# Kernel tuning notes

Hardware: AMD Instinct MI355X
Metric: run time of the kernel (lower is better)

## Reference

```python
import jax, jax.numpy as jnp
import numpy as np

# Model dims (GatedAttentionLayer of Qwen3.5 ANE hybrid stack)
C = 2048      # hidden_size
H = 16        # num_attention_heads
HK = 4        # num_key_value_heads
D = 128       # head_dim
ROT = 32      # rotary_dim = head_dim * partial_rotary_factor (0.25)
S = 1024      # sequence length (prefill)
CTX = 1024    # kv cache context length
N_ATTN = 6    # number of full-attention layers -> kv_cache leading dim 2*N_ATTN
EPS = 1e-6
ROPE_THETA = 1e7


def _rotate_half(x):
    h = x.shape[-1] // 2
    return jnp.concatenate([-x[..., h:], x[..., :h]], axis=-1)


def _rms_norm(x, w, eps=EPS):
    # Qwen3.5 convention: stored weight is (w - 1), applied as (1 + weight)
    r = jax.lax.rsqrt(jnp.mean(x * x, axis=-1, keepdims=True) + eps)
    return x * r * (1.0 + w)


def setup_inputs() -> dict:
    key = jax.random.key(0)
    ks = jax.random.split(key, 6)
    hidden_states = jax.random.normal(ks[0], (1, C, 1, S), jnp.float32)
    q_proj_w = jax.random.normal(ks[1], (H * 2 * D, C), jnp.float32) * 0.02  # q + gate
    k_proj_w = jax.random.normal(ks[2], (HK * D, C), jnp.float32) * 0.02
    v_proj_w = jax.random.normal(ks[3], (HK * D, C), jnp.float32) * 0.02
    o_proj_w = jax.random.normal(ks[4], (C, H * D), jnp.float32) * 0.02
    q_norm_w = jnp.zeros((D,), jnp.float32)
    k_norm_w = jnp.zeros((D,), jnp.float32)
    kv_cache = jnp.zeros((2 * N_ATTN, HK, CTX, D), jnp.float32)
    position_ids = jnp.arange(S, dtype=jnp.int32)
    # causal mask: 0 on/below diagonal, -1e9 above
    causal_mask = jnp.where(
        jnp.arange(CTX)[None, :] <= jnp.arange(S)[:, None], 0.0, -1e9
    ).astype(jnp.float32)[None, None]  # [1,1,S,CTX]
    # RoPE tables over rotary_dim
    inv_freq = 1.0 / (ROPE_THETA ** (jnp.arange(0, ROT, 2, dtype=jnp.float32) / ROT))
    t = jnp.arange(CTX, dtype=jnp.float32)
    freqs = jnp.outer(t, inv_freq)          # [CTX, ROT//2]
    emb = jnp.concatenate([freqs, freqs], -1)  # [CTX, ROT]
    cos_cached = jnp.cos(emb)
    sin_cached = jnp.sin(emb)
    return dict(hidden_states=hidden_states, q_proj_w=q_proj_w, k_proj_w=k_proj_w,
                v_proj_w=v_proj_w, o_proj_w=o_proj_w, q_norm_w=q_norm_w,
                k_norm_w=k_norm_w, kv_cache=kv_cache, causal_mask=causal_mask,
                position_ids=position_ids, cos_cached=cos_cached,
                sin_cached=sin_cached, attn_layer_idx=0)


def reference(hidden_states, q_proj_w, k_proj_w, v_proj_w, o_proj_w,
              q_norm_w, k_norm_w, kv_cache, causal_mask, position_ids,
              cos_cached, sin_cached, attn_layer_idx):
    x = hidden_states[0, :, 0, :]                     # [C, S]
    q_raw = q_proj_w @ x                              # [H*2D, S]  (1x1 Conv2d == GEMM)
    qg = q_raw.reshape(H, 2 * D, S)
    q = jnp.transpose(qg[:, :D, :], (0, 2, 1))        # [H, S, D]
    gate = jnp.transpose(qg[:, D:, :], (0, 2, 1))     # [H, S, D]
    k = jnp.transpose((k_proj_w @ x).reshape(HK, D, S), (0, 2, 1))  # [HK, S, D]
    v = jnp.transpose((v_proj_w @ x).reshape(HK, D, S), (0, 2, 1))  # [HK, S, D]

    q = _rms_norm(q, q_norm_w)
    k = _rms_norm(k, k_norm_w)

    cos = cos_cached[position_ids]   # [S, ROT]
    sin = sin_cached[position_ids]

    def rope(t):
        rot, pas = t[..., :ROT], t[..., ROT:]
        rot = rot * cos + _rotate_half(rot) * sin
        return jnp.concatenate([rot, pas], axis=-1)

    q, k = rope(q), rope(k)

    # prefill cache write at pos_start = position_ids[0]
    k_idx = 2 * attn_layer_idx
    v_idx = k_idx + 1
    pos_start = position_ids[0]
    kv_cache = jax.lax.dynamic_update_slice(kv_cache, k[None], (k_idx, 0, pos_start, 0))
    kv_cache = jax.lax.dynamic_update_slice(kv_cache, v[None], (v_idx, 0, pos_start, 0))

    g = H // HK  # GQA repeat (expand+reshape == contiguous repeat)
    k_full = jnp.repeat(kv_cache[k_idx], g, axis=0)   # [H, CTX, D]
    v_full = jnp.repeat(kv_cache[v_idx], g, axis=0)   # [H, CTX, D]

    scale = D ** -0.5
    attn = jnp.einsum('hsd,htd->hst', q, k_full) * scale + causal_mask[0]
    attn = jax.nn.softmax(attn, axis=-1)
    out = jnp.einsum('hst,htd->hsd', attn, v_full)    # [H, S, D]
    out = out * jax.nn.sigmoid(gate)
    out = jnp.transpose(out, (0, 2, 1)).reshape(H * D, S)
    output = (o_proj_w @ out)[None, :, None, :]       # [1, C, 1, S]
    return output
```

## Files before the change

kernel.cpp:

```cpp
#include <hip/hip_runtime.h>
#include <cstdint>

#define S_LEN 1024
#define C_DIM 2048
#define NH    16
#define NHK   4
#define HD    128
#define ROT   32
#define SCALE 0.08838834764831845f

typedef __bf16 bf16x8 __attribute__((ext_vector_type(8)));
typedef float floatx4 __attribute__((ext_vector_type(4)));
typedef float floatx16 __attribute__((ext_vector_type(16)));
typedef unsigned short ushortx8 __attribute__((ext_vector_type(8)));

__device__ __forceinline__ unsigned short f2bf(float f) {
  union { float f; uint32_t u; } x; x.f = f;
  uint32_t r = (x.u + 0x7fffu + ((x.u >> 16) & 1u)) >> 16;
  return (unsigned short)r;
}
__device__ __forceinline__ float bf2f(unsigned short v) {
  union { uint32_t u; float f; } x; x.u = (uint32_t)v << 16; return x.f;
}

__device__ __forceinline__ void async_copy16(const unsigned short* g, unsigned short* l) {
  __builtin_amdgcn_global_load_lds(
      (const __attribute__((address_space(1))) void*)g,
      (__attribute__((address_space(3))) void*)l,
      16, 0, 0);
}

__global__ void cast_all_kernel(const float* __restrict__ qw, const float* __restrict__ kw,
                                const float* __restrict__ vw, const float* __restrict__ ow,
                                unsigned short* __restrict__ out) {
  const int NQ = 4096 * 2048 / 4, NK = 512 * 2048 / 4, NV = 512 * 2048 / 4;
  int i = blockIdx.x * blockDim.x + threadIdx.x;
  const float* src; int j;
  if (i < NQ) { src = qw; j = i; }
  else if (i < NQ + NK) { src = kw; j = i - NQ; }
  else if (i < NQ + NK + NV) { src = vw; j = i - NQ - NK; }
  else { src = ow; j = i - NQ - NK - NV; }
  float4 v = ((const float4*)src)[j];
  ushort4 o;
  o.x = f2bf(v.x); o.y = f2bf(v.y); o.z = f2bf(v.z); o.w = f2bf(v.w);
  ((ushort4*)out)[i] = o;
}

__global__ __launch_bounds__(256)
void transpose_cast_x_kernel(const float* __restrict__ x, unsigned short* __restrict__ xT) {
  __shared__ float t[32][33];
  int st = blockIdx.x, ct = blockIdx.y;
  int c = threadIdx.x & 31, rq = threadIdx.x >> 5;
#pragma unroll
  for (int i = 0; i < 4; ++i) {
    int r = rq + i * 8;
    t[r][c] = x[(size_t)(ct * 32 + r) * S_LEN + st * 32 + c];
  }
  __syncthreads();
#pragma unroll
  for (int i = 0; i < 4; ++i) {
    int r = rq + i * 8;
    xT[(size_t)(st * 32 + r) * C_DIM + ct * 32 + c] = f2bf(t[c][r]);
  }
}

__device__ __forceinline__ void norm_rope_epi(
    floatx16 (&acc)[2], float (*pp)[32],
    const float* __restrict__ w, const int* __restrict__ pos_ids,
    const float* __restrict__ cosc, const float* __restrict__ sinc,
    unsigned short* __restrict__ outp,
    int wave, int lane, int wm, int scol0) {
  int l31 = lane & 31, half = lane >> 5;
  float s = 0.f;
#pragma unroll
  for (int mi = 0; mi < 2; ++mi)
#pragma unroll
    for (int reg = 0; reg < 16; ++reg) { float v = acc[mi][reg]; s += v * v; }
  s += __shfl_xor(s, 32);
  if (half == 0) pp[wave][l31] = s;
  __syncthreads();
  float rn = rsqrtf((pp[wave][l31] + pp[wave ^ 1][l31]) * (1.0f / 128.0f) + 1e-6f);
  int scol = scol0 + l31;
  int pos = pos_ids[scol];
#pragma unroll
  for (int mi = 0; mi < 2; ++mi) {
    bool rope = (wm == 0) && (mi == 0);
#pragma unroll
    for (int g = 0; g < 4; ++g) {
      int dbase = wm + mi * 32 + half * 4 + g * 8;
      ushort4 o;
#pragma unroll
      for (int rr = 0; rr < 4; ++rr) {
        int reg = g * 4 + rr;
        int d = dbase + rr;
        float v = acc[mi][reg] * rn * (1.0f + w[d]);
        if (rope) {
          float cv = cosc[pos * ROT + d], sv = sinc[pos * ROT + d];
          int d2 = (d < 16) ? d + 16 : d - 16;
          float pv = acc[mi][reg ^ 8] * rn * (1.0f + w[d2]);
          v = v * cv + ((d < 16) ? -pv : pv) * sv;
        }
        ((unsigned short*)&o)[rr] = f2bf(v);
      }
      *(ushort4*)&outp[(size_t)scol * HD + dbase] = o;
    }
  }
}

__global__ __launch_bounds__(256, 4)
void gemm_qkv_fused(const unsigned short* __restrict__ A,
                    const unsigned short* __restrict__ BT,
                    const float* __restrict__ qw, const float* __restrict__ kw,
                    const int* __restrict__ pos_ids,
                    const float* __restrict__ cosc, const float* __restrict__ sinc,
                    unsigned short* __restrict__ qb, unsigned short* __restrict__ kbuf,
                    unsigned short* __restrict__ vTb, unsigned short* __restrict__ sgb) {
  __shared__ unsigned short Asm[2][128 * 64];
  __shared__ unsigned short Bsm[2][64 * 64];
  __shared__ float pp[4][32];
  int tid = threadIdx.x, wave = tid >> 6, lane = tid & 63;
  int l31 = lane & 31, half = lane >> 5;
  int wm = (wave & 1) * 64, wn = (wave >> 1) * 32;
  int m0 = blockIdx.x * 128, n0 = blockIdx.y * 64;
  int r8 = lane >> 3, c8 = lane & 7;
  int arow[4], brow[2], apos[4], bpos[2];
#pragma unroll
  for (int i = 0; i < 4; ++i) { arow[i] = wave * 32 + i * 8 + r8; apos[i] = c8 ^ (arow[i] & 7); }
#pragma unroll
  for (int i = 0; i < 2; ++i) { brow[i] = wave * 16 + i * 8 + r8; bpos[i] = c8 ^ (brow[i] & 7); }
  const unsigned short* Ag = A + (size_t)m0 * C_DIM;
  const unsigned short* Bg = BT + (size_t)n0 * C_DIM;
  floatx16 acc[2];
  acc[0] = (floatx16)0.f; acc[1] = (floatx16)0.f;
  ushortx8 rA[4], rB[2];

#pragma unroll
  for (int i = 0; i < 4; ++i) rA[i] = *(const ushortx8*)(Ag + (size_t)arow[i] * C_DIM + c8 * 8);
#pragma unroll
  for (int i = 0; i < 2; ++i) rB[i] = *(const ushortx8*)(Bg + (size_t)brow[i] * C_DIM + c8 * 8);
#pragma unroll
  for (int i = 0; i < 4; ++i) *(ushortx8*)&Asm[0][arow[i] * 64 + apos[i] * 8] = rA[i];
#pragma unroll
  for (int i = 0; i < 2; ++i) *(ushortx8*)&Bsm[0][brow[i] * 64 + bpos[i] * 8] = rB[i];
  __syncthreads();

  for (int t = 0; t < 32; ++t) {
    int b = t & 1;
    if (t < 31) {
      int kt = (t + 1) * 64;
#pragma unroll
      for (int i = 0; i < 4; ++i) rA[i] = *(const ushortx8*)(Ag + (size_t)arow[i] * C_DIM + kt + c8 * 8);
#pragma unroll
      for (int i = 0; i < 2; ++i) rB[i] = *(const ushortx8*)(Bg + (size_t)brow[i] * C_DIM + kt + c8 * 8);
    }
#pragma unroll
    for (int kb = 0; kb < 4; ++kb) {
      int co = (((kb << 1) | half) ^ (l31 & 7)) << 3;
      bf16x8 a0 = *(const bf16x8*)&Asm[b][(wm + l31) * 64 + co];
      bf16x8 a1 = *(const bf16x8*)&Asm[b][(wm + 32 + l31) * 64 + co];
      bf16x8 bf = *(const bf16x8*)&Bsm[b][(wn + l31) * 64 + co];
      acc[0] = __builtin_amdgcn_mfma_f32_32x32x16_bf16(a0, bf, acc[0], 0, 0, 0);
      acc[1] = __builtin_amdgcn_mfma_f32_32x32x16_bf16(a1, bf, acc[1], 0, 0, 0);
    }
    if (t < 31) {
#pragma unroll
      for (int i = 0; i < 4; ++i) *(ushortx8*)&Asm[b ^ 1][arow[i] * 64 + apos[i] * 8] = rA[i];
#pragma unroll
      for (int i = 0; i < 2; ++i) *(ushortx8*)&Bsm[b ^ 1][brow[i] * 64 + bpos[i] * 8] = rB[i];
    }
    __syncthreads();
  }

  int scol0 = n0 + wn;
  int ty = blockIdx.x;
  if (ty < 32) {
    int h = ty >> 1;
    if ((ty & 1) == 0) {
      norm_rope_epi(acc, pp, qw, pos_ids, cosc, sinc,
                    qb + (size_t)h * S_LEN * HD, wave, lane, wm, scol0);
    } else {
      int scol = scol0 + l31;
#pragma unroll
      for (int mi = 0; mi < 2; ++mi)
#pragma unroll
        for (int g = 0; g < 4; ++g) {
          int dbase = wm + mi * 32 + half * 4 + g * 8;
          ushort4 o;
#pragma unroll
          for (int rr = 0; rr < 4; ++rr)
            ((unsigned short*)&o)[rr] = f2bf(1.0f / (1.0f + __expf(-acc[mi][g * 4 + rr])));
          *(ushort4*)&sgb[((size_t)h * S_LEN + scol) * HD + dbase] = o;
        }
    }
  } else if (ty < 36) {
    int hk = ty - 32;
    norm_rope_epi(acc, pp, kw, pos_ids, cosc, sinc,
                  kbuf + (size_t)hk * S_LEN * HD, wave, lane, wm, scol0);
  } else {
    int hk = ty - 36;
#pragma unroll
    for (int mi = 0; mi < 2; ++mi)
#pragma unroll
      for (int reg = 0; reg < 16; ++reg) {
        int d = wm + mi * 32 + (reg & 3) + 8 * (reg >> 2) + 4 * half;
        vTb[(size_t)hk * HD * S_LEN + (size_t)d * S_LEN + scol0 + l31] = f2bf(acc[mi][reg]);
      }
  }
}

__global__ __launch_bounds__(256, 4)
void gemm_oproj(const unsigned short* __restrict__ A,
                const unsigned short* __restrict__ BT,
                float* __restrict__ C) {
  __shared__ unsigned short Asm[2][128 * 64];
  __shared__ unsigned short Bsm[2][64 * 64];
  int tid = threadIdx.x, wave = tid >> 6, lane = tid & 63;
  int l31 = lane & 31, half = lane >> 5;
  int wm = (wave & 1) * 64, wn = (wave >> 1) * 32;
  int m0 = blockIdx.x * 128, n0 = blockIdx.y * 64;
  int r8 = lane >> 3, c8 = lane & 7;
  int arow[4], brow[2], apos[4], bpos[2];
#pragma unroll
  for (int i = 0; i < 4; ++i) { arow[i] = wave * 32 + i * 8 + r8; apos[i] = c8 ^ (arow[i] & 7); }
#pragma unroll
  for (int i = 0; i < 2; ++i) { brow[i] = wave * 16 + i * 8 + r8; bpos[i] = c8 ^ (brow[i] & 7); }
  const unsigned short* Ag = A + (size_t)m0 * C_DIM;
  const unsigned short* Bg = BT + (size_t)n0 * C_DIM;
  floatx16 acc[2];
  acc[0] = (floatx16)0.f; acc[1] = (floatx16)0.f;
  ushortx8 rA[4], rB[2];

#pragma unroll
  for (int i = 0; i < 4; ++i) rA[i] = *(const ushortx8*)(Ag + (size_t)arow[i] * C_DIM + c8 * 8);
#pragma unroll
  for (int i = 0; i < 2; ++i) rB[i] = *(const ushortx8*)(Bg + (size_t)brow[i] * C_DIM + c8 * 8);
#pragma unroll
  for (int i = 0; i < 4; ++i) *(ushortx8*)&Asm[0][arow[i] * 64 + apos[i] * 8] = rA[i];
#pragma unroll
  for (int i = 0; i < 2; ++i) *(ushortx8*)&Bsm[0][brow[i] * 64 + bpos[i] * 8] = rB[i];
  __syncthreads();

  for (int t = 0; t < 32; ++t) {
    int b = t & 1;
    if (t < 31) {
      int kt = (t + 1) * 64;
#pragma unroll
      for (int i = 0; i < 4; ++i) rA[i] = *(const ushortx8*)(Ag + (size_t)arow[i] * C_DIM + kt + c8 * 8);
#pragma unroll
      for (int i = 0; i < 2; ++i) rB[i] = *(const ushortx8*)(Bg + (size_t)brow[i] * C_DIM + kt + c8 * 8);
    }
#pragma unroll
    for (int kb = 0; kb < 4; ++kb) {
      int co = (((kb << 1) | half) ^ (l31 & 7)) << 3;
      bf16x8 a0 = *(const bf16x8*)&Asm[b][(wm + l31) * 64 + co];
      bf16x8 a1 = *(const bf16x8*)&Asm[b][(wm + 32 + l31) * 64 + co];
      bf16x8 bf = *(const bf16x8*)&Bsm[b][(wn + l31) * 64 + co];
      acc[0] = __builtin_amdgcn_mfma_f32_32x32x16_bf16(a0, bf, acc[0], 0, 0, 0);
      acc[1] = __builtin_amdgcn_mfma_f32_32x32x16_bf16(a1, bf, acc[1], 0, 0, 0);
    }
    if (t < 31) {
#pragma unroll
      for (int i = 0; i < 4; ++i) *(ushortx8*)&Asm[b ^ 1][arow[i] * 64 + apos[i] * 8] = rA[i];
#pragma unroll
      for (int i = 0; i < 2; ++i) *(ushortx8*)&Bsm[b ^ 1][brow[i] * 64 + bpos[i] * 8] = rB[i];
    }
    __syncthreads();
  }
#pragma unroll
  for (int mi = 0; mi < 2; ++mi)
#pragma unroll
    for (int reg = 0; reg < 16; ++reg) {
      int row = m0 + wm + mi * 32 + (reg & 3) + 8 * (reg >> 2) + 4 * half;
      C[(size_t)row * S_LEN + n0 + wn + l31] = acc[mi][reg];
    }
}

__global__ __launch_bounds__(256)
void attn_kernel(const unsigned short* __restrict__ qb,
                 const unsigned short* __restrict__ kbuf,
                 const unsigned short* __restrict__ vTb,
                 const unsigned short* __restrict__ sgb,
                 unsigned short* __restrict__ outT) {
  __shared__ __align__(16) unsigned short Ks[64 * 128];
  __shared__ __align__(16) unsigned short Vs[128 * 64];
  __shared__ __align__(16) unsigned short Ps[4][16][72];
  int h = blockIdx.x, qt = blockIdx.y;
  int s0 = qt * 64;
  int hk = h >> 2;
  int tid = threadIdx.x, wave = tid >> 6, lane = tid & 63;
  int l16 = lane & 15, quad = lane >> 4;
  int lsw = l16 & 7;

  const unsigned short* qg = qb + ((size_t)(h * S_LEN + s0 + wave * 16 + l16)) * HD;
  bf16x8 qfr[4];
#pragma unroll
  for (int kb = 0; kb < 4; ++kb)
    qfr[kb] = *(const bf16x8*)(qg + kb * 32 + quad * 8);

  float m_r[4], l_r[4];
#pragma unroll
  for (int r = 0; r < 4; ++r) { m_r[r] = -1e30f; l_r[r] = 0.f; }
  floatx4 acc_o[8];
#pragma unroll
  for (int i = 0; i < 8; ++i) acc_o[i] = (floatx4)0.f;
  int srow_base = s0 + wave * 16 + quad * 4;

  const unsigned short* kg0 = kbuf + (size_t)hk * S_LEN * HD;
  const unsigned short* vg0 = vTb + (size_t)hk * HD * S_LEN;

  int kr4 = lane >> 4, kc16 = lane & 15;
  int vr8 = lane >> 3, vc8 = lane & 7;

  for (int t = 0; t <= qt; ++t) {
    int jt = t * 64;
#pragma unroll
    for (int i = 0; i < 4; ++i) {
      int rbase = wave * 16 + i * 4;
      int row = rbase + kr4;
      int cs = kc16 ^ (row & 7);
      async_copy16(kg0 + (size_t)(jt + row) * HD + cs * 8, Ks + rbase * 128);
    }
#pragma unroll
    for (int i = 0; i < 4; ++i) {
      int rbase = wave * 32 + i * 8;
      int row = rbase + vr8;
      int cs = vc8 ^ (row & 7);
      async_copy16(vg0 + (size_t)row * S_LEN + jt + cs * 8, Vs + rbase * 64);
    }
    __syncthreads();

    floatx4 acc_s[4];
#pragma unroll
    for (int ni = 0; ni < 4; ++ni) acc_s[ni] = (floatx4)0.f;
#pragma unroll
    for (int kb = 0; kb < 4; ++kb) {
#pragma unroll
      for (int ni = 0; ni < 4; ++ni) {
        int cl = (kb * 4 + quad) ^ lsw;
        bf16x8 bk = *(const bf16x8*)&Ks[(ni * 16 + l16) * 128 + cl * 8];
        acc_s[ni] = __builtin_amdgcn_mfma_f32_16x16x32_bf16(qfr[kb], bk, acc_s[ni], 0, 0, 0);
      }
    }

    bool diag = (t == qt);
    float alpha[4];
#pragma unroll
    for (int r = 0; r < 4; ++r) {
      float scv[4];
      float mx = -1e30f;
#pragma unroll
      for (int ni = 0; ni < 4; ++ni) {
        float sv = acc_s[ni][r] * SCALE;
        if (diag) {
          int jg = jt + ni * 16 + l16;
          if (jg > srow_base + r) sv = -1e30f;
        }
        scv[ni] = sv;
        mx = fmaxf(mx, sv);
      }
#pragma unroll
      for (int off = 8; off; off >>= 1) mx = fmaxf(mx, __shfl_xor(mx, off, 16));
      float mnew = fmaxf(m_r[r], mx);
      float psv = 0.f;
#pragma unroll
      for (int ni = 0; ni < 4; ++ni) {
        float pv = (scv[ni] > -1e29f) ? __expf(scv[ni] - mnew) : 0.f;
        Ps[wave][quad * 4 + r][ni * 16 + l16] = f2bf(pv);
        psv += pv;
      }
#pragma unroll
      for (int off = 8; off; off >>= 1) psv += __shfl_xor(psv, off, 16);
      alpha[r] = __expf(m_r[r] - mnew);
      m_r[r] = mnew;
      l_r[r] = l_r[r] * alpha[r] + psv;
    }
#pragma unroll
    for (int i = 0; i < 8; ++i)
#pragma unroll
      for (int r = 0; r < 4; ++r) acc_o[i][r] *= alpha[r];
    __threadfence_block();

#pragma unroll
    for (int kb2 = 0; kb2 < 2; ++kb2) {
      bf16x8 ap = *(const bf16x8*)&Ps[wave][l16][kb2 * 32 + quad * 8];
#pragma unroll
      for (int ni2 = 0; ni2 < 8; ++ni2) {
        int cl = (kb2 * 4 + quad) ^ lsw;
        bf16x8 bv = *(const bf16x8*)&Vs[(ni2 * 16 + l16) * 64 + cl * 8];
        acc_o[ni2] = __builtin_amdgcn_mfma_f32_16x16x32_bf16(ap, bv, acc_o[ni2], 0, 0, 0);
      }
    }
    __syncthreads();
  }

#pragma unroll
  for (int r = 0; r < 4; ++r) {
    int s = srow_base + r;
    float inv = 1.0f / l_r[r];
    const unsigned short* sgp = sgb + ((size_t)h * S_LEN + s) * HD;
    unsigned short* op = outT + (size_t)s * (NH * HD) + h * HD;
#pragma unroll
    for (int ni2 = 0; ni2 < 8; ++ni2) {
      int d = ni2 * 16 + l16;
      op[d] = f2bf(acc_o[ni2][r] * inv * bf2f(sgp[d]));
    }
  }
}

extern "C" void kernel_launch(void* const* d_in, const int* in_sizes, int n_in,
                              void* d_out, int out_size, void* d_ws, size_t ws_size,
                              hipStream_t stream) {
  const float* hs       = (const float*)d_in[0];
  const float* q_proj_w = (const float*)d_in[1];
  const float* k_proj_w = (const float*)d_in[2];
  const float* v_proj_w = (const float*)d_in[3];
  const float* o_proj_w = (const float*)d_in[4];
  const float* q_norm_w = (const float*)d_in[5];
  const float* k_norm_w = (const float*)d_in[6];
  const int*   pos_ids  = (const int*)d_in[9];
  const float* cos_c    = (const float*)d_in[10];
  const float* sin_c    = (const float*)d_in[11];
  float* out = (float*)d_out;

  char* ws = (char*)d_ws;
  unsigned short* wqkv = (unsigned short*)(ws + 0);
  unsigned short* wo   = (unsigned short*)(ws + 20971520);
  unsigned short* xT   = (unsigned short*)(ws + 29360128);
  unsigned short* qb   = (unsigned short*)(ws + 33554432);
  unsigned short* kbuf = (unsigned short*)(ws + 37748736);
  unsigned short* vTb  = (unsigned short*)(ws + 38797312);
  unsigned short* sgb  = (unsigned short*)(ws + 39845888);
  unsigned short* aoT  = (unsigned short*)(ws + 44040192);

  cast_all_kernel<<<14336, 256, 0, stream>>>(q_proj_w, k_proj_w, v_proj_w, o_proj_w, wqkv);
  transpose_cast_x_kernel<<<dim3(32, 64), 256, 0, stream>>>(hs, xT);
  gemm_qkv_fused<<<dim3(40, 16), 256, 0, stream>>>(wqkv, xT, q_norm_w, k_norm_w,
                                                   pos_ids, cos_c, sin_c,
                                                   qb, kbuf, vTb, sgb);
  attn_kernel<<<dim3(16, 16), 256, 0, stream>>>(qb, kbuf, vTb, sgb, aoT);
  gemm_oproj<<<dim3(16, 16), 256, 0, stream>>>(wo, aoT, out);
}
```

Measured before the change: 246.7 us.

## Fuse weight bf16 casts into GEMM loaders and double-buffer attention K/V loads

Removes the separate weight-cast kernel. Both GEMMs now load fp32 weights directly and convert them to bf16 in registers before the LDS store, which avoids writing and re-reading a bf16 weight copy. The GEMM barriers become an LDS-only wait plus s_barrier. The attention kernel double-buffers the K tiles and issues async K/V prefetches with explicit vmcnt waits, overlapping the loads with the MFMA work. In exchange, each GEMM block reads twice as many bytes for A, and correctness depends on hand-counted vmcnt values.

```diff
diff --git a/kernel.cpp b/kernel.cpp
--- a/kernel.cpp
+++ b/kernel.cpp
@@ -11,6 +11,7 @@
 
 typedef __bf16 bf16x8 __attribute__((ext_vector_type(8)));
 typedef float floatx4 __attribute__((ext_vector_type(4)));
+typedef float floatx8 __attribute__((ext_vector_type(8)));
 typedef float floatx16 __attribute__((ext_vector_type(16)));
 typedef unsigned short ushortx8 __attribute__((ext_vector_type(8)));
 
@@ -21,6 +22,12 @@
 }
 __device__ __forceinline__ float bf2f(unsigned short v) {
   union { uint32_t u; float f; } x; x.u = (uint32_t)v << 16; return x.f;
+}
+__device__ __forceinline__ ushortx8 cvt8(floatx8 v) {
+  ushortx8 o;
+#pragma unroll
+  for (int j = 0; j < 8; ++j) o[j] = f2bf(v[j]);
+  return o;
 }
 
 __device__ __forceinline__ void async_copy16(const unsigned short* g, unsigned short* l) {
@@ -30,20 +37,11 @@
       16, 0, 0);
 }
 
-__global__ void cast_all_kernel(const float* __restrict__ qw, const float* __restrict__ kw,
-                                const float* __restrict__ vw, const float* __restrict__ ow,
-                                unsigned short* __restrict__ out) {
-  const int NQ = 4096 * 2048 / 4, NK = 512 * 2048 / 4, NV = 512 * 2048 / 4;
-  int i = blockIdx.x * blockDim.x + threadIdx.x;
-  const float* src; int j;
-  if (i < NQ) { src = qw; j = i; }
-  else if (i < NQ + NK) { src = kw; j = i - NQ; }
-  else if (i < NQ + NK + NV) { src = vw; j = i - NQ - NK; }
-  else { src = ow; j = i - NQ - NK - NV; }
-  float4 v = ((const float4*)src)[j];
-  ushort4 o;
-  o.x = f2bf(v.x); o.y = f2bf(v.y); o.z = f2bf(v.z); o.w = f2bf(v.w);
-  ((ushort4*)out)[i] = o;
+#define WAIT_VM(N) asm volatile("s_waitcnt vmcnt(" #N ")" ::: "memory")
+
+__device__ __forceinline__ void bar_lds_only() {
+  asm volatile("s_waitcnt lgkmcnt(0)" ::: "memory");
+  __builtin_amdgcn_s_barrier();
 }
 
 __global__ __launch_bounds__(256)
@@ -107,10 +105,24 @@
   }
 }
 
+#define MFMA_PHASE(BUF)                                                            \
+  {                                                                                \
+    _Pragma("unroll")                                                              \
+    for (int kb = 0; kb < 4; ++kb) {                                               \
+      int co = (((kb << 1) | half) ^ (l31 & 7)) << 3;                              \
+      bf16x8 a0 = *(const bf16x8*)&Asm[BUF][(wm + l31) * 64 + co];                 \
+      bf16x8 a1 = *(const bf16x8*)&Asm[BUF][(wm + 32 + l31) * 64 + co];            \
+      bf16x8 bf = *(const bf16x8*)&Bsm[BUF][(wn + l31) * 64 + co];                 \
+      acc[0] = __builtin_amdgcn_mfma_f32_32x32x16_bf16(a0, bf, acc[0], 0, 0, 0);   \
+      acc[1] = __builtin_amdgcn_mfma_f32_32x32x16_bf16(a1, bf, acc[1], 0, 0, 0);   \
+    }                                                                              \
+  }
+
 __global__ __launch_bounds__(256, 4)
-void gemm_qkv_fused(const unsigned short* __restrict__ A,
+void gemm_qkv_fused(const float* __restrict__ qpw, const float* __restrict__ kpw,
+                    const float* __restrict__ vpw,
                     const unsigned short* __restrict__ BT,
-                    const float* __restrict__ qw, const float* __restrict__ kw,
+                    const float* __restrict__ qnw, const float* __restrict__ knw,
                     const int* __restrict__ pos_ids,
                     const float* __restrict__ cosc, const float* __restrict__ sinc,
                     unsigned short* __restrict__ qb, unsigned short* __restrict__ kbuf,
@@ -128,55 +140,50 @@
   for (int i = 0; i < 4; ++i) { arow[i] = wave * 32 + i * 8 + r8; apos[i] = c8 ^ (arow[i] & 7); }
 #pragma unroll
   for (int i = 0; i < 2; ++i) { brow[i] = wave * 16 + i * 8 + r8; bpos[i] = c8 ^ (brow[i] & 7); }
-  const unsigned short* Ag = A + (size_t)m0 * C_DIM;
+  int ty = blockIdx.x;
+  const float* Agf;
+  if (ty < 32)      Agf = qpw + (size_t)m0 * C_DIM;
+  else if (ty < 36) Agf = kpw + (size_t)(m0 - 4096) * C_DIM;
+  else              Agf = vpw + (size_t)(m0 - 4608) * C_DIM;
   const unsigned short* Bg = BT + (size_t)n0 * C_DIM;
   floatx16 acc[2];
   acc[0] = (floatx16)0.f; acc[1] = (floatx16)0.f;
-  ushortx8 rA[4], rB[2];
-
-#pragma unroll
-  for (int i = 0; i < 4; ++i) rA[i] = *(const ushortx8*)(Ag + (size_t)arow[i] * C_DIM + c8 * 8);
+  floatx8 fA[4]; ushortx8 rB[2];
+
+#pragma unroll
+  for (int i = 0; i < 4; ++i) fA[i] = *(const floatx8*)(Agf + (size_t)arow[i] * C_DIM + c8 * 8);
 #pragma unroll
   for (int i = 0; i < 2; ++i) rB[i] = *(const ushortx8*)(Bg + (size_t)brow[i] * C_DIM + c8 * 8);
 #pragma unroll
-  for (int i = 0; i < 4; ++i) *(ushortx8*)&Asm[0][arow[i] * 64 + apos[i] * 8] = rA[i];
+  for (int i = 0; i < 4; ++i) *(ushortx8*)&Asm[0][arow[i] * 64 + apos[i] * 8] = cvt8(fA[i]);
 #pragma unroll
   for (int i = 0; i < 2; ++i) *(ushortx8*)&Bsm[0][brow[i] * 64 + bpos[i] * 8] = rB[i];
-  __syncthreads();
+  bar_lds_only();
 
   for (int t = 0; t < 32; ++t) {
     int b = t & 1;
     if (t < 31) {
       int kt = (t + 1) * 64;
 #pragma unroll
-      for (int i = 0; i < 4; ++i) rA[i] = *(const ushortx8*)(Ag + (size_t)arow[i] * C_DIM + kt + c8 * 8);
+      for (int i = 0; i < 4; ++i) fA[i] = *(const floatx8*)(Agf + (size_t)arow[i] * C_DIM + kt + c8 * 8);
 #pragma unroll
       for (int i = 0; i < 2; ++i) rB[i] = *(const ushortx8*)(Bg + (size_t)brow[i] * C_DIM + kt + c8 * 8);
     }
-#pragma unroll
-    for (int kb = 0; kb < 4; ++kb) {
-      int co = (((kb << 1) | half) ^ (l31 & 7)) << 3;
-      bf16x8 a0 = *(const bf16x8*)&Asm[b][(wm + l31) * 64 + co];
-      bf16x8 a1 = *(const bf16x8*)&Asm[b][(wm + 32 + l31) * 64 + co];
-      bf16x8 bf = *(const bf16x8*)&Bsm[b][(wn + l31) * 64 + co];
-      acc[0] = __builtin_amdgcn_mfma_f32_32x32x16_bf16(a0, bf, acc[0], 0, 0, 0);
-      acc[1] = __builtin_amdgcn_mfma_f32_32x32x16_bf16(a1, bf, acc[1], 0, 0, 0);
-    }
+    if (b == 0) { MFMA_PHASE(0) } else { MFMA_PHASE(1) }
     if (t < 31) {
 #pragma unroll
-      for (int i = 0; i < 4; ++i) *(ushortx8*)&Asm[b ^ 1][arow[i] * 64 + apos[i] * 8] = rA[i];
+      for (int i = 0; i < 4; ++i) *(ushortx8*)&Asm[b ^ 1][arow[i] * 64 + apos[i] * 8] = cvt8(fA[i]);
 #pragma unroll
       for (int i = 0; i < 2; ++i) *(ushortx8*)&Bsm[b ^ 1][brow[i] * 64 + bpos[i] * 8] = rB[i];
     }
-    __syncthreads();
+    bar_lds_only();
   }
 
   int scol0 = n0 + wn;
-  int ty = blockIdx.x;
   if (ty < 32) {
     int h = ty >> 1;
     if ((ty & 1) == 0) {
-      norm_rope_epi(acc, pp, qw, pos_ids, cosc, sinc,
+      norm_rope_epi(acc, pp, qnw, pos_ids, cosc, sinc,
                     qb + (size_t)h * S_LEN * HD, wave, lane, wm, scol0);
     } else {
       int scol = scol0 + l31;
@@ -194,7 +201,7 @@
     }
   } else if (ty < 36) {
     int hk = ty - 32;
-    norm_rope_epi(acc, pp, kw, pos_ids, cosc, sinc,
+    norm_rope_epi(acc, pp, knw, pos_ids, cosc, sinc,
                   kbuf + (size_t)hk * S_LEN * HD, wave, lane, wm, scol0);
   } else {
     int hk = ty - 36;
@@ -209,7 +216,7 @@
 }
 
 __global__ __launch_bounds__(256, 4)
-void gemm_oproj(const unsigned short* __restrict__ A,
+void gemm_oproj(const float* __restrict__ A,
                 const unsigned short* __restrict__ BT,
                 float* __restrict__ C) {
   __shared__ unsigned short Asm[2][128 * 64];
@@ -224,47 +231,39 @@
   for (int i = 0; i < 4; ++i) { arow[i] = wave * 32 + i * 8 + r8; apos[i] = c8 ^ (arow[i] & 7); }
 #pragma unroll
   for (int i = 0; i < 2; ++i) { brow[i] = wave * 16 + i * 8 + r8; bpos[i] = c8 ^ (brow[i] & 7); }
-  const unsigned short* Ag = A + (size_t)m0 * C_DIM;
+  const float* Ag = A + (size_t)m0 * C_DIM;
   const unsigned short* Bg = BT + (size_t)n0 * C_DIM;
   floatx16 acc[2];
   acc[0] = (floatx16)0.f; acc[1] = (floatx16)0.f;
-  ushortx8 rA[4], rB[2];
-
-#pragma unroll
-  for (int i = 0; i < 4; ++i) rA[i] = *(const ushortx8*)(Ag + (size_t)arow[i] * C_DIM + c8 * 8);
+  floatx8 fA[4]; ushortx8 rB[2];
+
+#pragma unroll
+  for (int i = 0; i < 4; ++i) fA[i] = *(const floatx8*)(Ag + (size_t)arow[i] * C_DIM + c8 * 8);
 #pragma unroll
   for (int i = 0; i < 2; ++i) rB[i] = *(const ushortx8*)(Bg + (size_t)brow[i] * C_DIM + c8 * 8);
 #pragma unroll
-  for (int i = 0; i < 4; ++i) *(ushortx8*)&Asm[0][arow[i] * 64 + apos[i] * 8] = rA[i];
+  for (int i = 0; i < 4; ++i) *(ushortx8*)&Asm[0][arow[i] * 64 + apos[i] * 8] = cvt8(fA[i]);
 #pragma unroll
   for (int i = 0; i < 2; ++i) *(ushortx8*)&Bsm[0][brow[i] * 64 + bpos[i] * 8] = rB[i];
-  __syncthreads();
+  bar_lds_only();
 
   for (int t = 0; t < 32; ++t) {
     int b = t & 1;
     if (t < 31) {
       int kt = (t + 1) * 64;
 #pragma unroll
-      for (int i = 0; i < 4; ++i) rA[i] = *(const ushortx8*)(Ag + (size_t)arow[i] * C_DIM + kt + c8 * 8);
+      for (int i = 0; i < 4; ++i) fA[i] = *(const floatx8*)(Ag + (size_t)arow[i] * C_DIM + kt + c8 * 8);
 #pragma unroll
       for (int i = 0; i < 2; ++i) rB[i] = *(const ushortx8*)(Bg + (size_t)brow[i] * C_DIM + kt + c8 * 8);
     }
-#pragma unroll
-    for (int kb = 0; kb < 4; ++kb) {
-      int co = (((kb << 1) | half) ^ (l31 & 7)) << 3;
-      bf16x8 a0 = *(const bf16x8*)&Asm[b][(wm + l31) * 64 + co];
-      bf16x8 a1 = *(const bf16x8*)&Asm[b][(wm + 32 + l31) * 64 + co];
-      bf16x8 bf = *(const bf16x8*)&Bsm[b][(wn + l31) * 64 + co];
-      acc[0] = __builtin_amdgcn_mfma_f32_32x32x16_bf16(a0, bf, acc[0], 0, 0, 0);
-      acc[1] = __builtin_amdgcn_mfma_f32_32x32x16_bf16(a1, bf, acc[1], 0, 0, 0);
-    }
+    if (b == 0) { MFMA_PHASE(0) } else { MFMA_PHASE(1) }
     if (t < 31) {
 #pragma unroll
-      for (int i = 0; i < 4; ++i) *(ushortx8*)&Asm[b ^ 1][arow[i] * 64 + apos[i] * 8] = rA[i];
+      for (int i = 0; i < 4; ++i) *(ushortx8*)&Asm[b ^ 1][arow[i] * 64 + apos[i] * 8] = cvt8(fA[i]);
 #pragma unroll
       for (int i = 0; i < 2; ++i) *(ushortx8*)&Bsm[b ^ 1][brow[i] * 64 + bpos[i] * 8] = rB[i];
     }
-    __syncthreads();
+    bar_lds_only();
   }
 #pragma unroll
   for (int mi = 0; mi < 2; ++mi)
@@ -281,7 +280,7 @@
                  const unsigned short* __restrict__ vTb,
                  const unsigned short* __restrict__ sgb,
                  unsigned short* __restrict__ outT) {
-  __shared__ __align__(16) unsigned short Ks[64 * 128];
+  __shared__ __align__(16) unsigned short Ks[2][64 * 128];
   __shared__ __align__(16) unsigned short Vs[128 * 64];
   __shared__ __align__(16) unsigned short Ps[4][16][72];
   int h = blockIdx.x, qt = blockIdx.y;
@@ -296,6 +295,8 @@
 #pragma unroll
   for (int kb = 0; kb < 4; ++kb)
     qfr[kb] = *(const bf16x8*)(qg + kb * 32 + quad * 8);
+  asm volatile("" :: "v"(qfr[0]), "v"(qfr[1]), "v"(qfr[2]), "v"(qfr[3]));
+  WAIT_VM(0);
 
   float m_r[4], l_r[4];
 #pragma unroll
@@ -311,23 +312,32 @@
   int kr4 = lane >> 4, kc16 = lane & 15;
   int vr8 = lane >> 3, vc8 = lane & 7;
 
+#define STAGE_K(BUF, T)                                                    \
+  { _Pragma("unroll")                                                      \
+    for (int i = 0; i < 4; ++i) {                                          \
+      int rbase = wave * 16 + i * 4;                                       \
+      int row = rbase + kr4;                                               \
+      int cs = kc16 ^ (row & 7);                                           \
+      async_copy16(kg0 + (size_t)((T) * 64 + row) * HD + cs * 8,           \
+                   &Ks[BUF][rbase * 128]); } }
+#define STAGE_V(T)                                                         \
+  { _Pragma("unroll")                                                      \
+    for (int i = 0; i < 4; ++i) {                                          \
+      int rbase = wave * 32 + i * 8;                                       \
+      int row = rbase + vr8;                                               \
+      int cs = vc8 ^ (row & 7);                                            \
+      async_copy16(vg0 + (size_t)row * S_LEN + (T) * 64 + cs * 8,          \
+                   Vs + rbase * 64); } }
+
+  STAGE_K(0, 0)
+  STAGE_V(0)
+
   for (int t = 0; t <= qt; ++t) {
-    int jt = t * 64;
-#pragma unroll
-    for (int i = 0; i < 4; ++i) {
-      int rbase = wave * 16 + i * 4;
-      int row = rbase + kr4;
-      int cs = kc16 ^ (row & 7);
-      async_copy16(kg0 + (size_t)(jt + row) * HD + cs * 8, Ks + rbase * 128);
-    }
-#pragma unroll
-    for (int i = 0; i < 4; ++i) {
-      int rbase = wave * 32 + i * 8;
-      int row = rbase + vr8;
-      int cs = vc8 ^ (row & 7);
-      async_copy16(vg0 + (size_t)row * S_LEN + jt + cs * 8, Vs + rbase * 64);
-    }
-    __syncthreads();
+    int cur = t & 1;
+    bool more = (t < qt);
+    if (more) { STAGE_K(cur ^ 1, t + 1) WAIT_VM(8); }
+    else      { WAIT_VM(4); }
+    __builtin_amdgcn_s_barrier();
 
     floatx4 acc_s[4];
 #pragma unroll
@@ -337,11 +347,12 @@
 #pragma unroll
       for (int ni = 0; ni < 4; ++ni) {
         int cl = (kb * 4 + quad) ^ lsw;
-        bf16x8 bk = *(const bf16x8*)&Ks[(ni * 16 + l16) * 128 + cl * 8];
+        bf16x8 bk = *(const bf16x8*)&Ks[cur][(ni * 16 + l16) * 128 + cl * 8];
         acc_s[ni] = __builtin_amdgcn_mfma_f32_16x16x32_bf16(qfr[kb], bk, acc_s[ni], 0, 0, 0);
       }
     }
 
+    int jt = t * 64;
     bool diag = (t == qt);
     float alpha[4];
 #pragma unroll
@@ -378,7 +389,10 @@
     for (int i = 0; i < 8; ++i)
 #pragma unroll
       for (int r = 0; r < 4; ++r) acc_o[i][r] *= alpha[r];
-    __threadfence_block();
+
+    if (more) { WAIT_VM(4); }
+    else      { WAIT_VM(0); }
+    __builtin_amdgcn_s_barrier();
 
 #pragma unroll
     for (int kb2 = 0; kb2 < 2; ++kb2) {
@@ -390,7 +404,8 @@
         acc_o[ni2] = __builtin_amdgcn_mfma_f32_16x16x32_bf16(ap, bv, acc_o[ni2], 0, 0, 0);
       }
     }
-    __syncthreads();
+    __builtin_amdgcn_s_barrier();
+    if (more) { STAGE_V(t + 1) }
   }
 
 #pragma unroll
@@ -405,6 +420,8 @@
       op[d] = f2bf(acc_o[ni2][r] * inv * bf2f(sgp[d]));
     }
   }
+#undef STAGE_K
+#undef STAGE_V
 }
 
 extern "C" void kernel_launch(void* const* d_in, const int* in_sizes, int n_in,
@@ -423,20 +440,18 @@
   float* out = (float*)d_out;
 
   char* ws = (char*)d_ws;
-  unsigned short* wqkv = (unsigned short*)(ws + 0);
-  unsigned short* wo   = (unsigned short*)(ws + 20971520);
-  unsigned short* xT   = (unsigned short*)(ws + 29360128);
-  unsigned short* qb   = (unsigned short*)(ws + 33554432);
-  unsigned short* kbuf = (unsigned short*)(ws + 37748736);
-  unsigned short* vTb  = (unsigned short*)(ws + 38797312);
-  unsigned short* sgb  = (unsigned short*)(ws + 39845888);
-  unsigned short* aoT  = (unsigned short*)(ws + 44040192);
-
-  cast_all_kernel<<<14336, 256, 0, stream>>>(q_proj_w, k_proj_w, v_proj_w, o_proj_w, wqkv);
+  unsigned short* xT   = (unsigned short*)(ws + 0);
+  unsigned short* qb   = (unsigned short*)(ws + 4194304);
+  unsigned short* kbuf = (unsigned short*)(ws + 8388608);
+  unsigned short* vTb  = (unsigned short*)(ws + 9437184);
+  unsigned short* sgb  = (unsigned short*)(ws + 10485760);
+  unsigned short* aoT  = (unsigned short*)(ws + 14680064);
+
   transpose_cast_x_kernel<<<dim3(32, 64), 256, 0, stream>>>(hs, xT);
-  gemm_qkv_fused<<<dim3(40, 16), 256, 0, stream>>>(wqkv, xT, q_norm_w, k_norm_w,
+  gemm_qkv_fused<<<dim3(40, 16), 256, 0, stream>>>(q_proj_w, k_proj_w, v_proj_w, xT,
+                                                   q_norm_w, k_norm_w,
                                                    pos_ids, cos_c, sin_c,
                                                    qb, kbuf, vTb, sgb);
   attn_kernel<<<dim3(16, 16), 256, 0, stream>>>(qb, kbuf, vTb, sgb, aoT);
-  gemm_oproj<<<dim3(16, 16), 256, 0, stream>>>(wo, aoT, out);
-}
+  gemm_oproj<<<dim3(16, 16), 256, 0, stream>>>(o_proj_w, aoT, out);
+}
```

Measured after the change: 266.6 us. +8.1%, slower.
